# Kernel optimization log

Hardware: AMD Instinct MI355X
Metric: run time of the kernel (lower is better)

## Reference

```python
import jax, jax.numpy as jnp
import numpy as np

S, T, B, IN, H, O = 64, 32, 512, 66, 1024, 1024  # S == max_length


def _gru_cell(x, h, Wih, Whh, bih, bhh):
    # PyTorch GRU cell: gates ordered (r, z, n)
    gi = x @ Wih.T + bih            # [B, 3H]
    gh = h @ Whh.T + bhh            # [B, 3H]
    ir, iz, inn = jnp.split(gi, 3, axis=1)
    hr, hz, hn = jnp.split(gh, 3, axis=1)
    r = jax.nn.sigmoid(ir + hr)
    z = jax.nn.sigmoid(iz + hz)
    n = jnp.tanh(inn + r * hn)
    return (1.0 - z) * n + z * h


def setup_inputs() -> dict:
    key = jax.random.key(0)
    ks = jax.random.split(key, 20)
    s = 0.02
    return {
        "input_tensor": jax.random.normal(ks[0], (S, B, IN), jnp.float32),
        "target_tensor": jax.random.normal(ks[1], (T, B, H), jnp.float32),
        # encoder GRU
        "enc_Wih": jax.random.normal(ks[2], (3 * H, IN), jnp.float32) * s,
        "enc_Whh": jax.random.normal(ks[3], (3 * H, H), jnp.float32) * s,
        "enc_bih": jax.random.normal(ks[4], (3 * H,), jnp.float32) * s,
        "enc_bhh": jax.random.normal(ks[5], (3 * H,), jnp.float32) * s,
        # attention: Linear(2H -> max_length)
        "attn_W": jax.random.normal(ks[6], (S, 2 * H), jnp.float32) * s,
        "attn_b": jax.random.normal(ks[7], (S,), jnp.float32) * s,
        # attn_combine: Linear(2H -> H)
        "comb_W": jax.random.normal(ks[8], (H, 2 * H), jnp.float32) * s,
        "comb_b": jax.random.normal(ks[9], (H,), jnp.float32) * s,
        # decoder GRU
        "dec_Wih": jax.random.normal(ks[10], (3 * H, H), jnp.float32) * s,
        "dec_Whh": jax.random.normal(ks[11], (3 * H, H), jnp.float32) * s,
        "dec_bih": jax.random.normal(ks[12], (3 * H,), jnp.float32) * s,
        "dec_bhh": jax.random.normal(ks[13], (3 * H,), jnp.float32) * s,
        # output: Linear(H -> O)
        "out_W": jax.random.normal(ks[14], (O, H), jnp.float32) * s,
        "out_b": jax.random.normal(ks[15], (O,), jnp.float32) * s,
    }


def reference(input_tensor, target_tensor, enc_Wih, enc_Whh, enc_bih, enc_bhh,
              attn_W, attn_b, comb_W, comb_b, dec_Wih, dec_Whh, dec_bih,
              dec_bhh, out_W, out_b):
    batch = input_tensor.shape[1]
    h0 = jnp.zeros((batch, enc_Whh.shape[1]), input_tensor.dtype)

    # ---- encoder GRU over time ----
    def enc_step(h, x):
        h2 = _gru_cell(x, h, enc_Wih, enc_Whh, enc_bih, enc_bhh)
        return h2, h2

    enc_h, enc_out = jax.lax.scan(enc_step, h0, input_tensor)  # enc_out: [S, B, H]

    # ---- attention decoder, teacher forcing; loop t = 1..T-1 uses target[t-1] ----
    def dec_step(h, x):
        aw = jax.nn.softmax(jnp.concatenate([x, h], axis=1) @ attn_W.T + attn_b,
                            axis=1)                              # [B, S]
        ctx = jnp.einsum('bl,lbh->bh', aw, enc_out)              # [B, H]
        comb = jax.nn.relu(jnp.concatenate([x, ctx], axis=1) @ comb_W.T + comb_b)
        h2 = _gru_cell(comb, h, dec_Wih, dec_Whh, dec_bih, dec_bhh)
        out = jax.nn.log_softmax(h2 @ out_W.T + out_b, axis=1)   # [B, O]
        return h2, out

    _, outs = jax.lax.scan(dec_step, enc_h, target_tensor[:-1])
    # original overwrites `outputs` every step -> only last step survives
    return outs[-1]
```

## Files before the change

### kernel.cpp

```cpp
#include <hip/hip_runtime.h>
#include <hip/hip_bf16.h>
#include <math.h>

#define S_LEN 64
#define T_LEN 32
#define BATCH 512
#define IN_DIM 66
#define INP 128
#define H_DIM 1024
#define O_DIM 1024
#define H3 3072

typedef __attribute__((ext_vector_type(8))) short short8;
typedef __attribute__((ext_vector_type(4))) float f32x4;
typedef __attribute__((ext_vector_type(4))) unsigned short us4;

__device__ __forceinline__ unsigned short f2b(float f) {
    union { float f; unsigned u; } x; x.f = f;
    unsigned r = x.u + 0x7FFF + ((x.u >> 16) & 1);
    return (unsigned short)(r >> 16);
}
__device__ __forceinline__ float b2f(unsigned short s) {
    union { unsigned u; float f; } x; x.u = ((unsigned)s) << 16;
    return x.f;
}
__device__ __forceinline__ void gll16(const void* g, const void* l) {
    __builtin_amdgcn_global_load_lds(
        (const __attribute__((address_space(1))) unsigned int*)g,
        (__attribute__((address_space(3))) unsigned int*)l, 16, 0, 0);
}

template<int TM, int TN>
__global__ __launch_bounds__(256) void gemm_k(
    const unsigned short* __restrict__ A, int lda,
    const unsigned short* __restrict__ W, int ldw,
    const float* __restrict__ bias,
    const float* __restrict__ addf, const unsigned short* __restrict__ addb,
    int ldadd,
    float* __restrict__ Cf,
    unsigned short* __restrict__ Cb, int ldc,
    int K, int flags)
{
    constexpr int IF = TM / 16;
    constexpr int JF = TN / 64;
    constexpr int NW = TN / 4;
    constexpr int CA = TM * 4;
    constexpr int CW = TN * 4;
    __shared__ __align__(16) unsigned short As[TM * 32];
    __shared__ __align__(16) unsigned short Bs[TN * 32];

    const int bm = blockIdx.y * TM;
    const int bn = blockIdx.x * TN;
    const int t = threadIdx.x;
    const int lane = t & 63;
    const int wv = t >> 6;
    const int ln = lane & 15;
    const int quad = lane >> 4;

    f32x4 acc[IF][JF];
    #pragma unroll
    for (int i = 0; i < IF; i++)
        #pragma unroll
        for (int j = 0; j < JF; j++) {
            f32x4 z = {0.f, 0.f, 0.f, 0.f};
            acc[i][j] = z;
        }

    for (int k0 = 0; k0 < K; k0 += 32) {
        if constexpr (CA >= 256) {
            #pragma unroll
            for (int j = 0; j < CA / 256; j++) {
                int ch = j * 256 + t;
                gll16(A + (size_t)(bm + (ch >> 2)) * lda + k0 + (ch & 3) * 8,
                      (const char*)As + (j * 4 + wv) * 1024);
            }
        } else {
            if (t < CA)
                gll16(A + (size_t)(bm + (t >> 2)) * lda + k0 + (t & 3) * 8,
                      (const char*)As + wv * 1024);
        }
        if constexpr (CW >= 256) {
            #pragma unroll
            for (int j = 0; j < CW / 256; j++) {
                int ch = j * 256 + t;
                gll16(W + (size_t)(bn + (ch >> 2)) * ldw + k0 + (ch & 3) * 8,
                      (const char*)Bs + (j * 4 + wv) * 1024);
            }
        } else {
            if (t < CW)
                gll16(W + (size_t)(bn + (t >> 2)) * ldw + k0 + (t & 3) * 8,
                      (const char*)Bs + wv * 1024);
        }
        __syncthreads();
        short8 af[IF], bf[JF];
        #pragma unroll
        for (int i = 0; i < IF; i++)
            af[i] = *(const short8*)&As[(i * 16 + ln) * 32 + quad * 8];
        #pragma unroll
        for (int j = 0; j < JF; j++)
            bf[j] = *(const short8*)&Bs[(wv * NW + j * 16 + ln) * 32 + quad * 8];
        #pragma unroll
        for (int i = 0; i < IF; i++)
            #pragma unroll
            for (int j = 0; j < JF; j++)
                acc[i][j] = __builtin_amdgcn_mfma_f32_16x16x32_bf16(
                    af[i], bf[j], acc[i][j], 0, 0, 0);
        __syncthreads();
    }

    #pragma unroll
    for (int i = 0; i < IF; i++) {
        #pragma unroll
        for (int j = 0; j < JF; j++) {
            #pragma unroll
            for (int r = 0; r < 4; r++) {
                int m = bm + i * 16 + quad * 4 + r;
                int n = bn + wv * NW + j * 16 + ln;
                float v = acc[i][j][r];
                if (flags & 1) v += bias[n];
                if (flags & 2) v += addf[(size_t)m * ldadd + n];
                if (flags & 4) v += b2f(addb[(size_t)m * ldadd + n]);
                if (flags & 8) v = fmaxf(v, 0.f);
                if (flags & 16) Cf[(size_t)m * ldc + n] = v;
                if (flags & 32) Cb[(size_t)m * ldc + n] = f2b(v);
            }
        }
    }
}

__device__ __forceinline__ void gru_tile(
    const unsigned short* __restrict__ A, int lda,
    const unsigned short* __restrict__ W, int ldw, int kb,
    unsigned short* As_g, unsigned short* Ws_g,
    int bm, int bn, int gt, int gwv, int ln, int quad,
    f32x4 (&accR)[2], f32x4 (&accZ)[2], f32x4 (&accN)[2])
{
    {
        int s = gt >> 7, r = (gt >> 2) & 31, c = gt & 3;
        gll16(A + (size_t)(bm + r) * lda + kb + s * 32 + c * 8,
              (const char*)As_g + gwv * 1024);
    }
    #pragma unroll
    for (int j = 0; j < 6; j++) {
        int ch = j * 256 + gt;
        int g2 = ch >> 9, ch2 = ch & 511;
        int s = ch2 >> 8, r = (ch2 >> 2) & 63, c = ch2 & 3;
        gll16(W + (size_t)(g2 * H_DIM + bn + r) * ldw + kb + s * 32 + c * 8,
              (const char*)Ws_g + j * 4096 + gwv * 1024);
    }
    __syncthreads();
    #pragma unroll
    for (int sub = 0; sub < 2; sub++) {
        short8 a[2], bw[3];
        #pragma unroll
        for (int i = 0; i < 2; i++)
            a[i] = *(const short8*)&As_g[sub * 1024 + (i * 16 + ln) * 32 + quad * 8];
        #pragma unroll
        for (int g = 0; g < 3; g++)
            bw[g] = *(const short8*)&Ws_g[g * 4096 + sub * 2048 + (gwv * 16 + ln) * 32 + quad * 8];
        #pragma unroll
        for (int i = 0; i < 2; i++) {
            accR[i] = __builtin_amdgcn_mfma_f32_16x16x32_bf16(a[i], bw[0], accR[i], 0, 0, 0);
            accZ[i] = __builtin_amdgcn_mfma_f32_16x16x32_bf16(a[i], bw[1], accZ[i], 0, 0, 0);
            accN[i] = __builtin_amdgcn_mfma_f32_16x16x32_bf16(a[i], bw[2], accN[i], 0, 0, 0);
        }
    }
    __syncthreads();
}

__global__ __launch_bounds__(512) void gru_gemm(
    const unsigned short* __restrict__ A0, int lda0,
    const unsigned short* __restrict__ W0, int ldw0, int K0,
    const unsigned short* __restrict__ A1,
    const unsigned short* __restrict__ W1,
    const float* __restrict__ bih, const float* __restrict__ bhh,
    const float* __restrict__ hf_in, float* __restrict__ hf_out,
    unsigned short* __restrict__ hb_out, unsigned short* __restrict__ slot)
{
    __shared__ __align__(16) unsigned short As2[2][2 * 32 * 32];
    __shared__ __align__(16) unsigned short Ws2[2][3 * 2 * 64 * 32];
    const int bm = blockIdx.y * 32;
    const int bn = blockIdx.x * 64;
    const int t = threadIdx.x;
    const int wg = t >> 8;
    const int gt = t & 255;
    const int lane = t & 63;
    const int gwv = gt >> 6;
    const int ln = lane & 15;
    const int quad = lane >> 4;

    unsigned short* As_g = As2[wg];
    unsigned short* Ws_g = Ws2[wg];

    f32x4 accR[2], accZ[2], accN0[2], accN1[2];
    #pragma unroll
    for (int i = 0; i < 2; i++) {
        f32x4 z = {0.f, 0.f, 0.f, 0.f};
        accR[i] = z; accZ[i] = z; accN0[i] = z; accN1[i] = z;
    }

    const int half0 = K0 >> 1;
    for (int k0 = 0; k0 < half0; k0 += 64)
        gru_tile(A0, lda0, W0, ldw0, wg * half0 + k0, As_g, Ws_g,
                 bm, bn, gt, gwv, ln, quad, accR, accZ, accN0);
    for (int k0 = 0; k0 < 512; k0 += 64)
        gru_tile(A1, H_DIM, W1, H_DIM, wg * 512 + k0, As_g, Ws_g,
                 bm, bn, gt, gwv, ln, quad, accR, accZ, accN1);

    float* red = (float*)Ws2;
    const int rb = (gwv * 64 + lane) * 33;
    if (wg == 1) {
        #pragma unroll
        for (int i = 0; i < 2; i++)
            #pragma unroll
            for (int r = 0; r < 4; r++) {
                red[rb + i * 4 + r]      = accR[i][r];
                red[rb + 8 + i * 4 + r]  = accZ[i][r];
                red[rb + 16 + i * 4 + r] = accN0[i][r];
                red[rb + 24 + i * 4 + r] = accN1[i][r];
            }
    }
    __syncthreads();
    if (wg == 0) {
        #pragma unroll
        for (int i = 0; i < 2; i++)
            #pragma unroll
            for (int r = 0; r < 4; r++) {
                accR[i][r]  += red[rb + i * 4 + r];
                accZ[i][r]  += red[rb + 8 + i * 4 + r];
                accN0[i][r] += red[rb + 16 + i * 4 + r];
                accN1[i][r] += red[rb + 24 + i * 4 + r];
            }
        const int n = bn + gwv * 16 + ln;
        const float br = bih[n] + bhh[n];
        const float bz = bih[H_DIM + n] + bhh[H_DIM + n];
        const float bi_n = bih[2 * H_DIM + n];
        const float bh_n = bhh[2 * H_DIM + n];
        #pragma unroll
        for (int i = 0; i < 2; i++) {
            #pragma unroll
            for (int r = 0; r < 4; r++) {
                const int m = bm + i * 16 + quad * 4 + r;
                const size_t idx = (size_t)m * H_DIM + n;
                float rg = 1.f / (1.f + __expf(-(accR[i][r] + br)));
                float zg = 1.f / (1.f + __expf(-(accZ[i][r] + bz)));
                float av = accN0[i][r] + bi_n + rg * (accN1[i][r] + bh_n);
                float e2 = __expf(-2.f * fabsf(av));
                float th = (1.f - e2) / (1.f + e2);
                th = av < 0.f ? -th : th;
                float o = (1.f - zg) * th + zg * hf_in[idx];
                hf_out[idx] = o;
                unsigned short ob = f2b(o);
                hb_out[idx] = ob;
                if (slot) slot[idx] = ob;
            }
        }
    }
}

__global__ __launch_bounds__(256) void attn_ctx(
    const unsigned short* __restrict__ hb,
    const unsigned short* __restrict__ wAhT,
    const unsigned short* __restrict__ attnx_t,
    const unsigned short* __restrict__ encb,
    unsigned short* __restrict__ ctx)
{
    __shared__ float hf[H_DIM];
    __shared__ float part[4][S_LEN];
    __shared__ float awl[S_LEN];
    const int b = blockIdx.x, t = threadIdx.x;
    {
        us4 u = *(const us4*)(hb + ((size_t)b << 10) + t * 4);
        #pragma unroll
        for (int j = 0; j < 4; j++) hf[t * 4 + j] = b2f(u[j]);
    }
    __syncthreads();
    {
        const int c = t & 63, ks = (t >> 6) * 256;
        float s = 0.f;
        #pragma unroll 8
        for (int k = 0; k < 256; k++)
            s += hf[ks + k] * b2f(wAhT[(size_t)(ks + k) * S_LEN + c]);
        part[t >> 6][c] = s;
    }
    __syncthreads();
    if (t < 64) {
        float v = part[0][t] + part[1][t] + part[2][t] + part[3][t]
                + b2f(attnx_t[b * S_LEN + t]);
        float m = v;
        #pragma unroll
        for (int off = 32; off; off >>= 1) m = fmaxf(m, __shfl_xor(m, off));
        float e = __expf(v - m);
        float ss = e;
        #pragma unroll
        for (int off = 32; off; off >>= 1) ss += __shfl_xor(ss, off);
        awl[t] = e / ss;
    }
    __syncthreads();
    const int hq = t * 4;
    float s0 = 0.f, s1 = 0.f, s2 = 0.f, s3 = 0.f;
    #pragma unroll 4
    for (int l = 0; l < S_LEN; l++) {
        us4 u = *(const us4*)(encb + (((size_t)l * BATCH + b) << 10) + hq);
        float w = awl[l];
        s0 += w * b2f(u[0]); s1 += w * b2f(u[1]);
        s2 += w * b2f(u[2]); s3 += w * b2f(u[3]);
    }
    us4 o; o[0] = f2b(s0); o[1] = f2b(s1); o[2] = f2b(s2); o[3] = f2b(s3);
    *(us4*)(ctx + ((size_t)b << 10) + hq) = o;
}

__global__ void cvt_w4(const float* __restrict__ src, int ld,
                       unsigned short* __restrict__ dst, int rows, int cols)
{
    int idx = blockIdx.x * blockDim.x + threadIdx.x;
    int total4 = rows * cols / 4;
    if (idx >= total4) return;
    int e = idx * 4;
    int r = e / cols, c = e - r * cols;
    const float* s = src + (size_t)r * ld + c;
    us4 o;
    #pragma unroll
    for (int j = 0; j < 4; j++) o[j] = f2b(s[j]);
    *(us4*)(dst + e) = o;
}

__global__ void cvt_plain4(const float* __restrict__ src,
                           unsigned short* __restrict__ dst, int total4)
{
    int idx = blockIdx.x * blockDim.x + threadIdx.x;
    if (idx >= total4) return;
    f32x4 v = *(const f32x4*)(src + (size_t)idx * 4);
    us4 o;
    #pragma unroll
    for (int j = 0; j < 4; j++) o[j] = f2b(v[j]);
    *(us4*)(dst + (size_t)idx * 4) = o;
}

__global__ void cvt_pad(const float* __restrict__ src, int scols,
                        unsigned short* __restrict__ dst, int dcols, int total)
{
    int idx = blockIdx.x * blockDim.x + threadIdx.x;
    if (idx >= total) return;
    int r = idx / dcols, c = idx - r * dcols;
    dst[idx] = (c < scols) ? f2b(src[(size_t)r * scols + c]) : (unsigned short)0;
}

__global__ void cvt_attT(const float* __restrict__ attn_W,
                         unsigned short* __restrict__ dst)
{
    int idx = blockIdx.x * blockDim.x + threadIdx.x;
    if (idx >= S_LEN * H_DIM) return;
    int k = idx >> 6, c = idx & 63;
    dst[idx] = f2b(attn_W[(size_t)c * 2 * H_DIM + H_DIM + k]);
}

__global__ void log_softmax1024(float* __restrict__ x)
{
    __shared__ float red[256];
    float* xr = x + (size_t)blockIdx.x * O_DIM;
    int t = threadIdx.x;
    float m = -1e30f;
    for (int i = t; i < O_DIM; i += 256) m = fmaxf(m, xr[i]);
    red[t] = m; __syncthreads();
    for (int s2 = 128; s2 > 0; s2 >>= 1) {
        if (t < s2) red[t] = fmaxf(red[t], red[t + s2]);
        __syncthreads();
    }
    m = red[0];
    __syncthreads();
    float s = 0.f;
    for (int i = t; i < O_DIM; i += 256) s += expf(xr[i] - m);
    red[t] = s; __syncthreads();
    for (int s2 = 128; s2 > 0; s2 >>= 1) {
        if (t < s2) red[t] += red[t + s2];
        __syncthreads();
    }
    float lse = m + logf(red[0]);
    __syncthreads();
    for (int i = t; i < O_DIM; i += 256) xr[i] = xr[i] - lse;
}

extern "C" void kernel_launch(void* const* d_in, const int* in_sizes, int n_in,
                              void* d_out, int out_size, void* d_ws, size_t ws_size,
                              hipStream_t stream)
{
    const float* input   = (const float*)d_in[0];
    const float* target  = (const float*)d_in[1];
    const float* enc_Wih = (const float*)d_in[2];
    const float* enc_Whh = (const float*)d_in[3];
    const float* enc_bih = (const float*)d_in[4];
    const float* enc_bhh = (const float*)d_in[5];
    const float* attn_W  = (const float*)d_in[6];
    const float* attn_b  = (const float*)d_in[7];
    const float* comb_W  = (const float*)d_in[8];
    const float* comb_b  = (const float*)d_in[9];
    const float* dec_Wih = (const float*)d_in[10];
    const float* dec_Whh = (const float*)d_in[11];
    const float* dec_bih = (const float*)d_in[12];
    const float* dec_bhh = (const float*)d_in[13];
    const float* out_W   = (const float*)d_in[14];
    const float* out_b   = (const float*)d_in[15];
    float* out = (float*)d_out;

    char* p = (char*)d_ws;
    auto alloc = [&](size_t bytes) {
        char* r = p; p += (bytes + 255) & ~(size_t)255; return r;
    };
    unsigned short* wWhh  = (unsigned short*)alloc((size_t)H3 * H_DIM * 2);
    unsigned short* wDih  = (unsigned short*)alloc((size_t)H3 * H_DIM * 2);
    unsigned short* wDhh  = (unsigned short*)alloc((size_t)H3 * H_DIM * 2);
    unsigned short* wCc   = (unsigned short*)alloc((size_t)H_DIM * H_DIM * 2);
    unsigned short* wCx   = (unsigned short*)alloc((size_t)H_DIM * H_DIM * 2);
    unsigned short* wO    = (unsigned short*)alloc((size_t)O_DIM * H_DIM * 2);
    unsigned short* wAhT  = (unsigned short*)alloc((size_t)H_DIM * S_LEN * 2);
    unsigned short* wAx   = (unsigned short*)alloc((size_t)S_LEN * H_DIM * 2);
    unsigned short* wIhp  = (unsigned short*)alloc((size_t)H3 * INP * 2);
    unsigned short* xbp   = (unsigned short*)alloc((size_t)S_LEN * BATCH * INP * 2);
    unsigned short* encb  = (unsigned short*)alloc((size_t)S_LEN * BATCH * H_DIM * 2);
    unsigned short* combx = (unsigned short*)alloc((size_t)(T_LEN - 1) * BATCH * H_DIM * 2);
    unsigned short* attnx = (unsigned short*)alloc((size_t)(T_LEN - 1) * BATCH * S_LEN * 2);
    float*          h     = (float*)alloc((size_t)BATCH * H_DIM * 4);
    unsigned short* hbA   = (unsigned short*)alloc((size_t)BATCH * H_DIM * 2);
    unsigned short* hbB   = (unsigned short*)alloc((size_t)BATCH * H_DIM * 2);
    unsigned short* ctx   = (unsigned short*)alloc((size_t)BATCH * H_DIM * 2);
    unsigned short* comb  = (unsigned short*)alloc((size_t)BATCH * H_DIM * 2);
    unsigned short* targetb = encb;

    const dim3 blk(256);

    hipMemsetAsync(h,   0, (size_t)BATCH * H_DIM * 4, stream);
    hipMemsetAsync(hbA, 0, (size_t)BATCH * H_DIM * 2, stream);

    cvt_w4<<<(H3 * H_DIM / 4 + 255) / 256, blk, 0, stream>>>(enc_Whh, H_DIM, wWhh, H3, H_DIM);
    cvt_w4<<<(H3 * H_DIM / 4 + 255) / 256, blk, 0, stream>>>(dec_Wih, H_DIM, wDih, H3, H_DIM);
    cvt_w4<<<(H3 * H_DIM / 4 + 255) / 256, blk, 0, stream>>>(dec_Whh, H_DIM, wDhh, H3, H_DIM);
    cvt_w4<<<(H_DIM * H_DIM / 4 + 255) / 256, blk, 0, stream>>>(comb_W + H_DIM, 2 * H_DIM, wCc, H_DIM, H_DIM);
    cvt_w4<<<(H_DIM * H_DIM / 4 + 255) / 256, blk, 0, stream>>>(comb_W, 2 * H_DIM, wCx, H_DIM, H_DIM);
    cvt_w4<<<(O_DIM * H_DIM / 4 + 255) / 256, blk, 0, stream>>>(out_W, H_DIM, wO, O_DIM, H_DIM);
    cvt_w4<<<(S_LEN * H_DIM / 4 + 255) / 256, blk, 0, stream>>>(attn_W, 2 * H_DIM, wAx, S_LEN, H_DIM);
    cvt_attT<<<(S_LEN * H_DIM + 255) / 256, blk, 0, stream>>>(attn_W, wAhT);
    cvt_pad<<<((S_LEN * BATCH * INP) + 255) / 256, blk, 0, stream>>>(
        input, IN_DIM, xbp, INP, S_LEN * BATCH * INP);
    cvt_pad<<<((H3 * INP) + 255) / 256, blk, 0, stream>>>(
        enc_Wih, IN_DIM, wIhp, INP, H3 * INP);
    cvt_plain4<<<((T_LEN * BATCH * H_DIM / 4) + 255) / 256, blk, 0, stream>>>(
        target, targetb, T_LEN * BATCH * H_DIM / 4);

    const int MT = (T_LEN - 1) * BATCH;
    gemm_k<64, 64><<<dim3(1, MT / 64), blk, 0, stream>>>(
        targetb, H_DIM, wAx, H_DIM, attn_b,
        nullptr, nullptr, 0, nullptr, attnx, S_LEN, H_DIM, 1 | 32);
    gemm_k<128, 128><<<dim3(H_DIM / 128, MT / 128), blk, 0, stream>>>(
        targetb, H_DIM, wCx, H_DIM, comb_b,
        nullptr, nullptr, 0, nullptr, combx, H_DIM, H_DIM, 1 | 32);

    const dim3 grid_gru(H_DIM / 64, BATCH / 32);
    const dim3 blk512(512);
    unsigned short* hcur = hbA;
    unsigned short* hnxt = hbB;

    for (int s = 0; s < S_LEN; s++) {
        gru_gemm<<<grid_gru, blk512, 0, stream>>>(
            xbp + (size_t)s * BATCH * INP, INP, wIhp, INP, INP,
            hcur, wWhh, enc_bih, enc_bhh, h, h, hnxt,
            encb + (size_t)s * BATCH * H_DIM);
        unsigned short* tmp = hcur; hcur = hnxt; hnxt = tmp;
    }

    for (int t = 0; t < T_LEN - 1; t++) {
        attn_ctx<<<BATCH, blk, 0, stream>>>(
            hcur, wAhT, attnx + (size_t)t * BATCH * S_LEN, encb, ctx);
        gemm_k<32, 64><<<dim3(H_DIM / 64, BATCH / 32), blk, 0, stream>>>(
            ctx, H_DIM, wCc, H_DIM, nullptr,
            nullptr, combx + (size_t)t * BATCH * H_DIM, H_DIM,
            nullptr, comb, H_DIM, H_DIM, 4 | 8 | 32);
        gru_gemm<<<grid_gru, blk512, 0, stream>>>(
            comb, H_DIM, wDih, H_DIM, H_DIM,
            hcur, wDhh, dec_bih, dec_bhh, h, h, hnxt, nullptr);
        unsigned short* tmp = hcur; hcur = hnxt; hnxt = tmp;
    }

    gemm_k<32, 64><<<dim3(O_DIM / 64, BATCH / 32), blk, 0, stream>>>(
        hcur, H_DIM, wO, H_DIM, out_b,
        nullptr, nullptr, 0, out, nullptr, O_DIM, H_DIM, 1 | 16);
    log_softmax1024<<<BATCH, blk, 0, stream>>>(out);
}
```

Before: 3.123 ms.

## Replace LDS-staged GRU GEMM with direct register-prefetched global loads

The fused GRU gate GEMM no longer stages A and W tiles through shared memory with two K-split workgroup halves and an LDS reduction. Each wave now loads MFMA fragments straight from global memory into registers, double-buffered across 32-wide K steps, over a 256-thread block covering a 64x32 output tile. This drops the barriers and the cross-half reduction but gives up shared-memory reuse of A and W between waves and uses strided 16-byte global loads. The precompute GEMM for the combine projection also gets a smaller 64x128 tile.

```diff
diff --git a/kernel.cpp b/kernel.cpp
--- a/kernel.cpp
+++ b/kernel.cpp
@@ -128,47 +128,57 @@
     }
 }
 
-__device__ __forceinline__ void gru_tile(
+__device__ __forceinline__ void gru_mma(
+    short8 a0, short8 a1, short8 b0, short8 b1, short8 b2,
+    f32x4 (&accR)[2], f32x4 (&accZ)[2], f32x4 (&accN)[2])
+{
+    accR[0] = __builtin_amdgcn_mfma_f32_16x16x32_bf16(a0, b0, accR[0], 0, 0, 0);
+    accR[1] = __builtin_amdgcn_mfma_f32_16x16x32_bf16(a1, b0, accR[1], 0, 0, 0);
+    accZ[0] = __builtin_amdgcn_mfma_f32_16x16x32_bf16(a0, b1, accZ[0], 0, 0, 0);
+    accZ[1] = __builtin_amdgcn_mfma_f32_16x16x32_bf16(a1, b1, accZ[1], 0, 0, 0);
+    accN[0] = __builtin_amdgcn_mfma_f32_16x16x32_bf16(a0, b2, accN[0], 0, 0, 0);
+    accN[1] = __builtin_amdgcn_mfma_f32_16x16x32_bf16(a1, b2, accN[1], 0, 0, 0);
+}
+
+__device__ __forceinline__ void gru_phase(
     const unsigned short* __restrict__ A, int lda,
-    const unsigned short* __restrict__ W, int ldw, int kb,
-    unsigned short* As_g, unsigned short* Ws_g,
-    int bm, int bn, int gt, int gwv, int ln, int quad,
+    const unsigned short* __restrict__ W, int ldw, int K,
+    int ar0, int ar1, int br0, int br1, int br2, int ko,
     f32x4 (&accR)[2], f32x4 (&accZ)[2], f32x4 (&accN)[2])
 {
-    {
-        int s = gt >> 7, r = (gt >> 2) & 31, c = gt & 3;
-        gll16(A + (size_t)(bm + r) * lda + kb + s * 32 + c * 8,
-              (const char*)As_g + gwv * 1024);
-    }
-    #pragma unroll
-    for (int j = 0; j < 6; j++) {
-        int ch = j * 256 + gt;
-        int g2 = ch >> 9, ch2 = ch & 511;
-        int s = ch2 >> 8, r = (ch2 >> 2) & 63, c = ch2 & 3;
-        gll16(W + (size_t)(g2 * H_DIM + bn + r) * ldw + kb + s * 32 + c * 8,
-              (const char*)Ws_g + j * 4096 + gwv * 1024);
-    }
-    __syncthreads();
-    #pragma unroll
-    for (int sub = 0; sub < 2; sub++) {
-        short8 a[2], bw[3];
-        #pragma unroll
-        for (int i = 0; i < 2; i++)
-            a[i] = *(const short8*)&As_g[sub * 1024 + (i * 16 + ln) * 32 + quad * 8];
-        #pragma unroll
-        for (int g = 0; g < 3; g++)
-            bw[g] = *(const short8*)&Ws_g[g * 4096 + sub * 2048 + (gwv * 16 + ln) * 32 + quad * 8];
-        #pragma unroll
-        for (int i = 0; i < 2; i++) {
-            accR[i] = __builtin_amdgcn_mfma_f32_16x16x32_bf16(a[i], bw[0], accR[i], 0, 0, 0);
-            accZ[i] = __builtin_amdgcn_mfma_f32_16x16x32_bf16(a[i], bw[1], accZ[i], 0, 0, 0);
-            accN[i] = __builtin_amdgcn_mfma_f32_16x16x32_bf16(a[i], bw[2], accN[i], 0, 0, 0);
-        }
-    }
-    __syncthreads();
-}
-
-__global__ __launch_bounds__(512) void gru_gemm(
+    const unsigned short* pa0 = A + (size_t)ar0 * lda + ko;
+    const unsigned short* pa1 = A + (size_t)ar1 * lda + ko;
+    const unsigned short* pw0 = W + (size_t)br0 * ldw + ko;
+    const unsigned short* pw1 = W + (size_t)br1 * ldw + ko;
+    const unsigned short* pw2 = W + (size_t)br2 * ldw + ko;
+
+#define GRU_LD(va0, va1, vb0, vb1, vb2, kk)            \
+    va0 = *(const short8*)(pa0 + (kk));                \
+    va1 = *(const short8*)(pa1 + (kk));                \
+    vb0 = *(const short8*)(pw0 + (kk));                \
+    vb1 = *(const short8*)(pw1 + (kk));                \
+    vb2 = *(const short8*)(pw2 + (kk));
+
+    short8 a0A, a1A, b0A, b1A, b2A;
+    short8 a0B, a1B, b0B, b1B, b2B;
+    short8 a0T, a1T, b0T, b1T, b2T;
+    GRU_LD(a0A, a1A, b0A, b1A, b2A, 0)
+    GRU_LD(a0B, a1B, b0B, b1B, b2B, 32)
+    int k = 0;
+    for (; k < K - 64; k += 64) {
+        GRU_LD(a0T, a1T, b0T, b1T, b2T, k + 64)
+        gru_mma(a0A, a1A, b0A, b1A, b2A, accR, accZ, accN);
+        a0A = a0T; a1A = a1T; b0A = b0T; b1A = b1T; b2A = b2T;
+        GRU_LD(a0T, a1T, b0T, b1T, b2T, k + 96)
+        gru_mma(a0B, a1B, b0B, b1B, b2B, accR, accZ, accN);
+        a0B = a0T; a1B = a1T; b0B = b0T; b1B = b1T; b2B = b2T;
+    }
+    gru_mma(a0A, a1A, b0A, b1A, b2A, accR, accZ, accN);
+    gru_mma(a0B, a1B, b0B, b1B, b2B, accR, accZ, accN);
+#undef GRU_LD
+}
+
+__global__ __launch_bounds__(256) void gru_gemm(
     const unsigned short* __restrict__ A0, int lda0,
     const unsigned short* __restrict__ W0, int ldw0, int K0,
     const unsigned short* __restrict__ A1,
@@ -177,20 +187,18 @@
     const float* __restrict__ hf_in, float* __restrict__ hf_out,
     unsigned short* __restrict__ hb_out, unsigned short* __restrict__ slot)
 {
-    __shared__ __align__(16) unsigned short As2[2][2 * 32 * 32];
-    __shared__ __align__(16) unsigned short Ws2[2][3 * 2 * 64 * 32];
-    const int bm = blockIdx.y * 32;
-    const int bn = blockIdx.x * 64;
     const int t = threadIdx.x;
-    const int wg = t >> 8;
-    const int gt = t & 255;
+    const int w = t >> 6;
     const int lane = t & 63;
-    const int gwv = gt >> 6;
     const int ln = lane & 15;
     const int quad = lane >> 4;
-
-    unsigned short* As_g = As2[wg];
-    unsigned short* Ws_g = Ws2[wg];
+    const int bm = blockIdx.y * 64 + (w >> 1) * 32;
+    const int cg = blockIdx.x * 32 + (w & 1) * 16;
+    const int ar0 = bm + ln, ar1 = bm + 16 + ln;
+    const int br0 = cg + ln;
+    const int br1 = H_DIM + cg + ln;
+    const int br2 = 2 * H_DIM + cg + ln;
+    const int ko = quad * 8;
 
     f32x4 accR[2], accZ[2], accN0[2], accN1[2];
     #pragma unroll
@@ -199,61 +207,33 @@
         accR[i] = z; accZ[i] = z; accN0[i] = z; accN1[i] = z;
     }
 
-    const int half0 = K0 >> 1;
-    for (int k0 = 0; k0 < half0; k0 += 64)
-        gru_tile(A0, lda0, W0, ldw0, wg * half0 + k0, As_g, Ws_g,
-                 bm, bn, gt, gwv, ln, quad, accR, accZ, accN0);
-    for (int k0 = 0; k0 < 512; k0 += 64)
-        gru_tile(A1, H_DIM, W1, H_DIM, wg * 512 + k0, As_g, Ws_g,
-                 bm, bn, gt, gwv, ln, quad, accR, accZ, accN1);
-
-    float* red = (float*)Ws2;
-    const int rb = (gwv * 64 + lane) * 33;
-    if (wg == 1) {
-        #pragma unroll
-        for (int i = 0; i < 2; i++)
-            #pragma unroll
-            for (int r = 0; r < 4; r++) {
-                red[rb + i * 4 + r]      = accR[i][r];
-                red[rb + 8 + i * 4 + r]  = accZ[i][r];
-                red[rb + 16 + i * 4 + r] = accN0[i][r];
-                red[rb + 24 + i * 4 + r] = accN1[i][r];
-            }
-    }
-    __syncthreads();
-    if (wg == 0) {
-        #pragma unroll
-        for (int i = 0; i < 2; i++)
-            #pragma unroll
-            for (int r = 0; r < 4; r++) {
-                accR[i][r]  += red[rb + i * 4 + r];
-                accZ[i][r]  += red[rb + 8 + i * 4 + r];
-                accN0[i][r] += red[rb + 16 + i * 4 + r];
-                accN1[i][r] += red[rb + 24 + i * 4 + r];
-            }
-        const int n = bn + gwv * 16 + ln;
-        const float br = bih[n] + bhh[n];
-        const float bz = bih[H_DIM + n] + bhh[H_DIM + n];
-        const float bi_n = bih[2 * H_DIM + n];
-        const float bh_n = bhh[2 * H_DIM + n];
-        #pragma unroll
-        for (int i = 0; i < 2; i++) {
-            #pragma unroll
-            for (int r = 0; r < 4; r++) {
-                const int m = bm + i * 16 + quad * 4 + r;
-                const size_t idx = (size_t)m * H_DIM + n;
-                float rg = 1.f / (1.f + __expf(-(accR[i][r] + br)));
-                float zg = 1.f / (1.f + __expf(-(accZ[i][r] + bz)));
-                float av = accN0[i][r] + bi_n + rg * (accN1[i][r] + bh_n);
-                float e2 = __expf(-2.f * fabsf(av));
-                float th = (1.f - e2) / (1.f + e2);
-                th = av < 0.f ? -th : th;
-                float o = (1.f - zg) * th + zg * hf_in[idx];
-                hf_out[idx] = o;
-                unsigned short ob = f2b(o);
-                hb_out[idx] = ob;
-                if (slot) slot[idx] = ob;
-            }
+    gru_phase(A0, lda0, W0, ldw0, K0, ar0, ar1, br0, br1, br2, ko,
+              accR, accZ, accN0);
+    gru_phase(A1, H_DIM, W1, H_DIM, H_DIM, ar0, ar1, br0, br1, br2, ko,
+              accR, accZ, accN1);
+
+    const int n = cg + ln;
+    const float br = bih[n] + bhh[n];
+    const float bz = bih[H_DIM + n] + bhh[H_DIM + n];
+    const float bi_n = bih[2 * H_DIM + n];
+    const float bh_n = bhh[2 * H_DIM + n];
+    #pragma unroll
+    for (int i = 0; i < 2; i++) {
+        #pragma unroll
+        for (int r = 0; r < 4; r++) {
+            const int m = bm + i * 16 + quad * 4 + r;
+            const size_t idx = (size_t)m * H_DIM + n;
+            float rg = 1.f / (1.f + __expf(-(accR[i][r] + br)));
+            float zg = 1.f / (1.f + __expf(-(accZ[i][r] + bz)));
+            float av = accN0[i][r] + bi_n + rg * (accN1[i][r] + bh_n);
+            float e2 = __expf(-2.f * fabsf(av));
+            float th = (1.f - e2) / (1.f + e2);
+            th = av < 0.f ? -th : th;
+            float o = (1.f - zg) * th + zg * hf_in[idx];
+            hf_out[idx] = o;
+            unsigned short ob = f2b(o);
+            hb_out[idx] = ob;
+            if (slot) slot[idx] = ob;
         }
     }
 }
@@ -451,17 +431,16 @@
     gemm_k<64, 64><<<dim3(1, MT / 64), blk, 0, stream>>>(
         targetb, H_DIM, wAx, H_DIM, attn_b,
         nullptr, nullptr, 0, nullptr, attnx, S_LEN, H_DIM, 1 | 32);
-    gemm_k<128, 128><<<dim3(H_DIM / 128, MT / 128), blk, 0, stream>>>(
+    gemm_k<64, 128><<<dim3(H_DIM / 128, MT / 64), blk, 0, stream>>>(
         targetb, H_DIM, wCx, H_DIM, comb_b,
         nullptr, nullptr, 0, nullptr, combx, H_DIM, H_DIM, 1 | 32);
 
-    const dim3 grid_gru(H_DIM / 64, BATCH / 32);
-    const dim3 blk512(512);
+    const dim3 grid_gru(H_DIM / 32, BATCH / 64);
     unsigned short* hcur = hbA;
     unsigned short* hnxt = hbB;
 
     for (int s = 0; s < S_LEN; s++) {
-        gru_gemm<<<grid_gru, blk512, 0, stream>>>(
+        gru_gemm<<<grid_gru, blk, 0, stream>>>(
             xbp + (size_t)s * BATCH * INP, INP, wIhp, INP, INP,
             hcur, wWhh, enc_bih, enc_bhh, h, h, hnxt,
             encb + (size_t)s * BATCH * H_DIM);
@@ -475,7 +454,7 @@
             ctx, H_DIM, wCc, H_DIM, nullptr,
             nullptr, combx + (size_t)t * BATCH * H_DIM, H_DIM,
             nullptr, comb, H_DIM, H_DIM, 4 | 8 | 32);
-        gru_gemm<<<grid_gru, blk512, 0, stream>>>(
+        gru_gemm<<<grid_gru, blk, 0, stream>>>(
             comb, H_DIM, wDih, H_DIM, H_DIM,
             hcur, wDhh, dec_bih, dec_bhh, h, h, hnxt, nullptr);
         unsigned short* tmp = hcur; hcur = hnxt; hnxt = tmp;
```

Result: slower. 4.234 ms (+35.6%).

## Replace split-K dual-group GRU GEMM with single-group double-buffered pipeline

Applied to the files above, without the earlier changes.

The GRU gate GEMM no longer splits K across two 256-thread groups with a shared-memory reduction. It now uses one 256-thread group that double-buffers the A and W tiles, issuing the next tile's loads before computing the current one. This removes the cross-group reduction and one barrier per tile, and overlaps loads with MFMA work, but each block now runs twice as many sequential K-steps with half the threads. The precompute GEMM for the combine-input projection also moves from 128x128 to 64x128 tiles.

```diff
diff --git a/kernel.cpp b/kernel.cpp
--- a/kernel.cpp
+++ b/kernel.cpp
@@ -128,36 +128,41 @@
     }
 }
 
-__device__ __forceinline__ void gru_tile(
+__device__ __forceinline__ void gru_issue(
     const unsigned short* __restrict__ A, int lda,
     const unsigned short* __restrict__ W, int ldw, int kb,
-    unsigned short* As_g, unsigned short* Ws_g,
-    int bm, int bn, int gt, int gwv, int ln, int quad,
-    f32x4 (&accR)[2], f32x4 (&accZ)[2], f32x4 (&accN)[2])
+    unsigned short* As_b, unsigned short* Ws_b,
+    int t, int wv, int bm, int bn)
 {
     {
-        int s = gt >> 7, r = (gt >> 2) & 31, c = gt & 3;
+        int s = t >> 7, r = (t >> 2) & 31, c = t & 3;
         gll16(A + (size_t)(bm + r) * lda + kb + s * 32 + c * 8,
-              (const char*)As_g + gwv * 1024);
+              (const char*)As_b + wv * 1024);
     }
     #pragma unroll
     for (int j = 0; j < 6; j++) {
-        int ch = j * 256 + gt;
+        int ch = j * 256 + t;
         int g2 = ch >> 9, ch2 = ch & 511;
         int s = ch2 >> 8, r = (ch2 >> 2) & 63, c = ch2 & 3;
         gll16(W + (size_t)(g2 * H_DIM + bn + r) * ldw + kb + s * 32 + c * 8,
-              (const char*)Ws_g + j * 4096 + gwv * 1024);
-    }
-    __syncthreads();
+              (const char*)Ws_b + j * 4096 + wv * 1024);
+    }
+}
+
+__device__ __forceinline__ void gru_compute(
+    const unsigned short* As_b, const unsigned short* Ws_b,
+    int wv, int ln, int quad,
+    f32x4 (&accR)[2], f32x4 (&accZ)[2], f32x4 (&accN)[2])
+{
     #pragma unroll
     for (int sub = 0; sub < 2; sub++) {
         short8 a[2], bw[3];
         #pragma unroll
         for (int i = 0; i < 2; i++)
-            a[i] = *(const short8*)&As_g[sub * 1024 + (i * 16 + ln) * 32 + quad * 8];
+            a[i] = *(const short8*)&As_b[sub * 1024 + (i * 16 + ln) * 32 + quad * 8];
         #pragma unroll
         for (int g = 0; g < 3; g++)
-            bw[g] = *(const short8*)&Ws_g[g * 4096 + sub * 2048 + (gwv * 16 + ln) * 32 + quad * 8];
+            bw[g] = *(const short8*)&Ws_b[g * 4096 + sub * 2048 + (wv * 16 + ln) * 32 + quad * 8];
         #pragma unroll
         for (int i = 0; i < 2; i++) {
             accR[i] = __builtin_amdgcn_mfma_f32_16x16x32_bf16(a[i], bw[0], accR[i], 0, 0, 0);
@@ -165,10 +170,9 @@
             accN[i] = __builtin_amdgcn_mfma_f32_16x16x32_bf16(a[i], bw[2], accN[i], 0, 0, 0);
         }
     }
-    __syncthreads();
-}
-
-__global__ __launch_bounds__(512) void gru_gemm(
+}
+
+__global__ __launch_bounds__(256) void gru_gemm(
     const unsigned short* __restrict__ A0, int lda0,
     const unsigned short* __restrict__ W0, int ldw0, int K0,
     const unsigned short* __restrict__ A1,
@@ -177,20 +181,15 @@
     const float* __restrict__ hf_in, float* __restrict__ hf_out,
     unsigned short* __restrict__ hb_out, unsigned short* __restrict__ slot)
 {
-    __shared__ __align__(16) unsigned short As2[2][2 * 32 * 32];
-    __shared__ __align__(16) unsigned short Ws2[2][3 * 2 * 64 * 32];
+    __shared__ __align__(16) unsigned short AsB[2][2 * 32 * 32];
+    __shared__ __align__(16) unsigned short WsB[2][3 * 2 * 64 * 32];
     const int bm = blockIdx.y * 32;
     const int bn = blockIdx.x * 64;
     const int t = threadIdx.x;
-    const int wg = t >> 8;
-    const int gt = t & 255;
     const int lane = t & 63;
-    const int gwv = gt >> 6;
+    const int wv = t >> 6;
     const int ln = lane & 15;
     const int quad = lane >> 4;
-
-    unsigned short* As_g = As2[wg];
-    unsigned short* Ws_g = Ws2[wg];
 
     f32x4 accR[2], accZ[2], accN0[2], accN1[2];
     #pragma unroll
@@ -199,61 +198,51 @@
         accR[i] = z; accZ[i] = z; accN0[i] = z; accN1[i] = z;
     }
 
-    const int half0 = K0 >> 1;
-    for (int k0 = 0; k0 < half0; k0 += 64)
-        gru_tile(A0, lda0, W0, ldw0, wg * half0 + k0, As_g, Ws_g,
-                 bm, bn, gt, gwv, ln, quad, accR, accZ, accN0);
-    for (int k0 = 0; k0 < 512; k0 += 64)
-        gru_tile(A1, H_DIM, W1, H_DIM, wg * 512 + k0, As_g, Ws_g,
-                 bm, bn, gt, gwv, ln, quad, accR, accZ, accN1);
-
-    float* red = (float*)Ws2;
-    const int rb = (gwv * 64 + lane) * 33;
-    if (wg == 1) {
-        #pragma unroll
-        for (int i = 0; i < 2; i++)
-            #pragma unroll
-            for (int r = 0; r < 4; r++) {
-                red[rb + i * 4 + r]      = accR[i][r];
-                red[rb + 8 + i * 4 + r]  = accZ[i][r];
-                red[rb + 16 + i * 4 + r] = accN0[i][r];
-                red[rb + 24 + i * 4 + r] = accN1[i][r];
-            }
-    }
-    __syncthreads();
-    if (wg == 0) {
-        #pragma unroll
-        for (int i = 0; i < 2; i++)
-            #pragma unroll
-            for (int r = 0; r < 4; r++) {
-                accR[i][r]  += red[rb + i * 4 + r];
-                accZ[i][r]  += red[rb + 8 + i * 4 + r];
-                accN0[i][r] += red[rb + 16 + i * 4 + r];
-                accN1[i][r] += red[rb + 24 + i * 4 + r];
-            }
-        const int n = bn + gwv * 16 + ln;
-        const float br = bih[n] + bhh[n];
-        const float bz = bih[H_DIM + n] + bhh[H_DIM + n];
-        const float bi_n = bih[2 * H_DIM + n];
-        const float bh_n = bhh[2 * H_DIM + n];
-        #pragma unroll
-        for (int i = 0; i < 2; i++) {
-            #pragma unroll
-            for (int r = 0; r < 4; r++) {
-                const int m = bm + i * 16 + quad * 4 + r;
-                const size_t idx = (size_t)m * H_DIM + n;
-                float rg = 1.f / (1.f + __expf(-(accR[i][r] + br)));
-                float zg = 1.f / (1.f + __expf(-(accZ[i][r] + bz)));
-                float av = accN0[i][r] + bi_n + rg * (accN1[i][r] + bh_n);
-                float e2 = __expf(-2.f * fabsf(av));
-                float th = (1.f - e2) / (1.f + e2);
-                th = av < 0.f ? -th : th;
-                float o = (1.f - zg) * th + zg * hf_in[idx];
-                hf_out[idx] = o;
-                unsigned short ob = f2b(o);
-                hb_out[idx] = ob;
-                if (slot) slot[idx] = ob;
-            }
+    const int nx0 = K0 >> 6;
+    const int NT = nx0 + 16;
+
+    gru_issue(A0, lda0, W0, ldw0, 0, AsB[0], WsB[0], t, wv, bm, bn);
+    for (int tl = 0; tl < NT; tl++) {
+        __syncthreads();
+        const int nxt = tl + 1;
+        if (nxt < NT) {
+            if (nxt < nx0)
+                gru_issue(A0, lda0, W0, ldw0, nxt << 6,
+                          AsB[nxt & 1], WsB[nxt & 1], t, wv, bm, bn);
+            else
+                gru_issue(A1, H_DIM, W1, H_DIM, (nxt - nx0) << 6,
+                          AsB[nxt & 1], WsB[nxt & 1], t, wv, bm, bn);
+        }
+        if (tl < nx0)
+            gru_compute(AsB[tl & 1], WsB[tl & 1], wv, ln, quad,
+                        accR, accZ, accN0);
+        else
+            gru_compute(AsB[tl & 1], WsB[tl & 1], wv, ln, quad,
+                        accR, accZ, accN1);
+    }
+
+    const int n = bn + wv * 16 + ln;
+    const float br = bih[n] + bhh[n];
+    const float bz = bih[H_DIM + n] + bhh[H_DIM + n];
+    const float bi_n = bih[2 * H_DIM + n];
+    const float bh_n = bhh[2 * H_DIM + n];
+    #pragma unroll
+    for (int i = 0; i < 2; i++) {
+        #pragma unroll
+        for (int r = 0; r < 4; r++) {
+            const int m = bm + i * 16 + quad * 4 + r;
+            const size_t idx = (size_t)m * H_DIM + n;
+            float rg = 1.f / (1.f + __expf(-(accR[i][r] + br)));
+            float zg = 1.f / (1.f + __expf(-(accZ[i][r] + bz)));
+            float av = accN0[i][r] + bi_n + rg * (accN1[i][r] + bh_n);
+            float e2 = __expf(-2.f * fabsf(av));
+            float th = (1.f - e2) / (1.f + e2);
+            th = av < 0.f ? -th : th;
+            float o = (1.f - zg) * th + zg * hf_in[idx];
+            hf_out[idx] = o;
+            unsigned short ob = f2b(o);
+            hb_out[idx] = ob;
+            if (slot) slot[idx] = ob;
         }
     }
 }
@@ -451,17 +440,16 @@
     gemm_k<64, 64><<<dim3(1, MT / 64), blk, 0, stream>>>(
         targetb, H_DIM, wAx, H_DIM, attn_b,
         nullptr, nullptr, 0, nullptr, attnx, S_LEN, H_DIM, 1 | 32);
-    gemm_k<128, 128><<<dim3(H_DIM / 128, MT / 128), blk, 0, stream>>>(
+    gemm_k<64, 128><<<dim3(H_DIM / 128, MT / 64), blk, 0, stream>>>(
         targetb, H_DIM, wCx, H_DIM, comb_b,
         nullptr, nullptr, 0, nullptr, combx, H_DIM, H_DIM, 1 | 32);
 
     const dim3 grid_gru(H_DIM / 64, BATCH / 32);
-    const dim3 blk512(512);
     unsigned short* hcur = hbA;
     unsigned short* hnxt = hbB;
 
     for (int s = 0; s < S_LEN; s++) {
-        gru_gemm<<<grid_gru, blk512, 0, stream>>>(
+        gru_gemm<<<grid_gru, blk, 0, stream>>>(
             xbp + (size_t)s * BATCH * INP, INP, wIhp, INP, INP,
             hcur, wWhh, enc_bih, enc_bhh, h, h, hnxt,
             encb + (size_t)s * BATCH * H_DIM);
@@ -475,7 +463,7 @@
             ctx, H_DIM, wCc, H_DIM, nullptr,
             nullptr, combx + (size_t)t * BATCH * H_DIM, H_DIM,
             nullptr, comb, H_DIM, H_DIM, 4 | 8 | 32);
-        gru_gemm<<<grid_gru, blk512, 0, stream>>>(
+        gru_gemm<<<grid_gru, blk, 0, stream>>>(
             comb, H_DIM, wDih, H_DIM, H_DIM,
             hcur, wDhh, dec_bih, dec_bhh, h, h, hnxt, nullptr);
         unsigned short* tmp = hcur; hcur = hnxt; hnxt = tmp;
```

New measurement: 3.782 ms. 21.1% more time.
